# Kernel optimization log

Measured on AMD Instinct MI355X. Metric: run time of the kernel, lower is better.

Reference implementation:

```python
import jax, jax.numpy as jnp
import numpy as np

D_MODEL = 512
N_HEADS = 4  # d_model >= 8 -> 4 heads
HEAD_DIM = D_MODEL // N_HEADS
D_FF = 4 * D_MODEL


def setup_inputs() -> dict:
    key = jax.random.key(0)
    ks = jax.random.split(key, 8)
    B, T = 4, 2048
    s = 0.02
    return {
        "x": jax.random.normal(ks[0], (B, T, D_MODEL), dtype=jnp.float32),
        "ln1_g": jnp.ones((D_MODEL,), jnp.float32),
        "ln1_b": jnp.zeros((D_MODEL,), jnp.float32),
        "w_qkv": jax.random.normal(ks[1], (D_MODEL, 3 * D_MODEL), jnp.float32) * s,
        "w_proj": jax.random.normal(ks[2], (D_MODEL, D_MODEL), jnp.float32) * s,
        "ln2_g": jnp.ones((D_MODEL,), jnp.float32),
        "ln2_b": jnp.zeros((D_MODEL,), jnp.float32),
        "w_ff1": jax.random.normal(ks[3], (D_MODEL, D_FF), jnp.float32) * s,
        "w_ff2": jax.random.normal(ks[4], (D_FF, D_MODEL), jnp.float32) * s,
    }


def _layernorm(x, g, b, eps=1e-5):
    mu = jnp.mean(x, axis=-1, keepdims=True)
    var = jnp.var(x, axis=-1, keepdims=True)
    return (x - mu) * jax.lax.rsqrt(var + eps) * g + b


def _attention(x, w_qkv, w_proj):
    B, T, C = x.shape
    qkv = x @ w_qkv  # [B,T,3C]
    q, k, v = jnp.split(qkv, 3, axis=-1)
    # [B,H,T,Dh]
    q = q.reshape(B, T, N_HEADS, HEAD_DIM).transpose(0, 2, 1, 3)
    k = k.reshape(B, T, N_HEADS, HEAD_DIM).transpose(0, 2, 1, 3)
    v = v.reshape(B, T, N_HEADS, HEAD_DIM).transpose(0, 2, 1, 3)
    scale = 1.0 / jnp.sqrt(jnp.asarray(HEAD_DIM, x.dtype))
    scores = jnp.einsum("bhqd,bhkd->bhqk", q, k) * scale
    causal = jnp.tril(jnp.ones((T, T), bool))
    scores = jnp.where(causal, scores, -jnp.inf)
    attn = jax.nn.softmax(scores, axis=-1)
    out = jnp.einsum("bhqk,bhkd->bhqd", attn, v)
    out = out.transpose(0, 2, 1, 3).reshape(B, T, C)
    return out @ w_proj


def reference(x, ln1_g, ln1_b, w_qkv, w_proj, ln2_g, ln2_b, w_ff1, w_ff2):
    x = x + _attention(_layernorm(x, ln1_g, ln1_b), w_qkv, w_proj)
    h = _layernorm(x, ln2_g, ln2_b)
    h = jax.nn.gelu(h @ w_ff1, approximate=False) @ w_ff2
    return x + h
```

## Files before the change

kernel.cpp:

```cpp
#include <hip/hip_runtime.h>
#include <cstdint>

typedef unsigned short u16;
typedef __attribute__((ext_vector_type(8))) short short8;
typedef __attribute__((ext_vector_type(4))) float floatx4;

#define BT    8192
#define TSEQ  2048
#define NBAT  4
#define CMOD  512
#define NH    4
#define HD    128
#define DFF   2048
#define CQKV  1536

__device__ __forceinline__ u16 f2bf(float f) {
  union { float f; uint32_t u; } v; v.f = f;
  uint32_t r = v.u + 0x7FFFu + ((v.u >> 16) & 1u);
  return (u16)(r >> 16);
}

__device__ __forceinline__ float exp2a(float x) {
  float r; asm("v_exp_f32 %0, %1" : "=v"(r) : "v"(x)); return r;
}
__device__ __forceinline__ float rcpa(float x) {
  float r; asm("v_rcp_f32 %0, %1" : "=v"(r) : "v"(x)); return r;
}

typedef __attribute__((address_space(1))) const unsigned int ga_u32;
typedef __attribute__((address_space(3))) unsigned int ls_u32;
__device__ __forceinline__ void glds16(const u16* g, u16* l) {
  __builtin_amdgcn_global_load_lds((ga_u32*)g, (ls_u32*)l, 16, 0, 0);
}

__global__ __launch_bounds__(256) void transpose_cast(const float* __restrict__ W,
                                                      u16* __restrict__ Wt, int K, int N) {
  __shared__ float tile[32][33];
  int n0 = blockIdx.x * 32, k0 = blockIdx.y * 32;
  int tx = threadIdx.x & 31, ty = threadIdx.x >> 5;
  #pragma unroll
  for (int r = 0; r < 32; r += 8)
    tile[r + ty][tx] = W[(size_t)(k0 + r + ty) * N + n0 + tx];
  __syncthreads();
  #pragma unroll
  for (int r = 0; r < 32; r += 8)
    Wt[(size_t)(n0 + r + ty) * K + k0 + tx] = f2bf(tile[tx][r + ty]);
}

__global__ __launch_bounds__(256) void ln_kernel(const float* __restrict__ x,
                                                 const float* __restrict__ g,
                                                 const float* __restrict__ b,
                                                 u16* __restrict__ out) {
  int row = blockIdx.x * 4 + (threadIdx.x >> 6);
  int lane = threadIdx.x & 63;
  const float4* xr = (const float4*)(x + (size_t)row * CMOD);
  float4 a = xr[lane], c = xr[lane + 64];
  float s = a.x + a.y + a.z + a.w + c.x + c.y + c.z + c.w;
  float q = a.x*a.x + a.y*a.y + a.z*a.z + a.w*a.w
          + c.x*c.x + c.y*c.y + c.z*c.z + c.w*c.w;
  #pragma unroll
  for (int o = 32; o; o >>= 1) { s += __shfl_xor(s, o); q += __shfl_xor(q, o); }
  float mu = s * (1.0f / CMOD);
  float rstd = rsqrtf(q * (1.0f / CMOD) - mu * mu + 1e-5f);
  const float4* gr = (const float4*)g;
  const float4* br = (const float4*)b;
  float4 g0 = gr[lane], g1 = gr[lane + 64], b0 = br[lane], b1 = br[lane + 64];
  u16* orow = out + (size_t)row * CMOD;
  int i0 = lane * 4, i1 = (lane + 64) * 4;
  orow[i0 + 0] = f2bf((a.x - mu) * rstd * g0.x + b0.x);
  orow[i0 + 1] = f2bf((a.y - mu) * rstd * g0.y + b0.y);
  orow[i0 + 2] = f2bf((a.z - mu) * rstd * g0.z + b0.z);
  orow[i0 + 3] = f2bf((a.w - mu) * rstd * g0.w + b0.w);
  orow[i1 + 0] = f2bf((c.x - mu) * rstd * g1.x + b1.x);
  orow[i1 + 1] = f2bf((c.y - mu) * rstd * g1.y + b1.y);
  orow[i1 + 2] = f2bf((c.z - mu) * rstd * g1.z + b1.z);
  orow[i1 + 3] = f2bf((c.w - mu) * rstd * g1.w + b1.w);
}

template <int EPI, int TN>
__global__ __launch_bounds__(256) void gemm_kernel(
    const u16* __restrict__ A, const u16* __restrict__ Bt, int K,
    const float* __restrict__ resid, float* __restrict__ outf,
    u16* __restrict__ ob0, u16* __restrict__ ob1, u16* __restrict__ ob2) {
  constexpr int WNF = TN / 32;
  constexpr int NKB = TN / 64;
  __shared__ __align__(16) u16 As[2][128 * 32];
  __shared__ __align__(16) u16 Bs[2][TN * 32];
  int tid = threadIdx.x;
  int lane = tid & 63, wave = tid >> 6;
  int lane16 = lane & 15, quad = lane >> 4;
  int m0 = blockIdx.y * 128, n0 = blockIdx.x * TN;
  int wm = (wave >> 1) * 64, wn = (wave & 1) * (TN / 2);

  floatx4 acc[4][WNF];
  #pragma unroll
  for (int i = 0; i < 4; i++)
    #pragma unroll
    for (int j = 0; j < WNF; j++) acc[i][j] = (floatx4)(0.0f);

  const u16* agp[2]; u16* alp[2][2];
  const u16* bgp[NKB]; u16* blp[NKB][2];
  #pragma unroll
  for (int i = 0; i < 2; i++) {
    int s = i * 256 + tid;
    agp[i] = A + (size_t)(m0 + (s >> 2)) * K + (s & 3) * 8;
    alp[i][0] = &As[0][(i * 256 + wave * 64) * 8];
    alp[i][1] = &As[1][(i * 256 + wave * 64) * 8];
  }
  #pragma unroll
  for (int i = 0; i < NKB; i++) {
    int s = i * 256 + tid;
    bgp[i] = Bt + (size_t)(n0 + (s >> 2)) * K + (s & 3) * 8;
    blp[i][0] = &Bs[0][(i * 256 + wave * 64) * 8];
    blp[i][1] = &Bs[1][(i * 256 + wave * 64) * 8];
  }

  int nk = K >> 5;
  #pragma unroll
  for (int i = 0; i < 2; i++) glds16(agp[i], alp[i][0]);
  #pragma unroll
  for (int i = 0; i < NKB; i++) glds16(bgp[i], blp[i][0]);

  for (int kt = 0; kt < nk; kt++) {
    __syncthreads();
    int buf = kt & 1;
    if (kt + 1 < nk) {
      int k1 = (kt + 1) * 32;
      #pragma unroll
      for (int i = 0; i < 2; i++) glds16(agp[i] + k1, alp[i][buf ^ 1]);
      #pragma unroll
      for (int i = 0; i < NKB; i++) glds16(bgp[i] + k1, blp[i][buf ^ 1]);
    }
    short8 af[4], bf[WNF];
    #pragma unroll
    for (int i = 0; i < 4; i++)
      af[i] = *(const short8*)&As[buf][(wm + i * 16 + lane16) * 32 + quad * 8];
    #pragma unroll
    for (int j = 0; j < WNF; j++)
      bf[j] = *(const short8*)&Bs[buf][(wn + j * 16 + lane16) * 32 + quad * 8];
    #pragma unroll
    for (int i = 0; i < 4; i++)
      #pragma unroll
      for (int j = 0; j < WNF; j++)
        acc[i][j] = __builtin_amdgcn_mfma_f32_16x16x32_bf16(af[i], bf[j], acc[i][j], 0, 0, 0);
  }

  #pragma unroll
  for (int i = 0; i < 4; i++) {
    #pragma unroll
    for (int j = 0; j < WNF; j++) {
      #pragma unroll
      for (int r = 0; r < 4; r++) {
        int m = m0 + wm + i * 16 + quad * 4 + r;
        int n = n0 + wn + j * 16 + lane16;
        float v = acc[i][j][r];
        if (EPI == 0) {
          int bb = m >> 11, t = m & 2047;
          int nn = n & 511, which = n >> 9;
          int h = nn >> 7, d = nn & 127;
          size_t bh = (size_t)(bb * NH + h);
          if (which == 0)      ob0[bh * TSEQ * HD + (size_t)t * HD + d] = f2bf(v * 0.12751743f);
          else if (which == 1) ob1[bh * TSEQ * HD + (size_t)t * HD + d] = f2bf(v);
          else                 ob2[bh * HD * TSEQ + (size_t)d * TSEQ + t] = f2bf(v);
        } else if (EPI == 1) {
          size_t idx = (size_t)m * CMOD + n;
          outf[idx] = v + resid[idx];
        } else if (EPI == 2) {
          float ge = 0.5f * v * (1.0f + erff(v * 0.70710678118654752f));
          ob0[(size_t)m * DFF + n] = f2bf(ge);
        } else {
          size_t idx = (size_t)m * CMOD + n;
          outf[idx] = v + resid[idx];
        }
      }
    }
  }
}

__global__ __launch_bounds__(256) void attn_kernel(const u16* __restrict__ qb,
                                                   const u16* __restrict__ kb,
                                                   const u16* __restrict__ vtb,
                                                   u16* __restrict__ ob) {
  __shared__ __align__(16) u16 Ks[2][32 * 128];
  __shared__ __align__(16) u16 Vs[2][128 * 32];
  __shared__ __align__(16) uint32_t Ps[4 * 16 * 20];
  int tid = threadIdx.x, wave = tid >> 6, lane = tid & 63;
  int lane16 = lane & 15, quad = lane >> 4;
  int bh = blockIdx.x;
  int qt = 31 - (int)blockIdx.y;
  int q0w = qt * 64 + wave * 16;
  const u16* Q  = qb  + (size_t)bh * TSEQ * HD;
  const u16* Kg = kb  + (size_t)bh * TSEQ * HD;
  const u16* Vg = vtb + (size_t)bh * HD * TSEQ;

  short8 aq[4];
  {
    int qrow = q0w + lane16;
    #pragma unroll
    for (int cc = 0; cc < 4; cc++)
      aq[cc] = *(const short8*)&Q[(size_t)qrow * HD + cc * 32 + quad * 8];
  }

  const u16* kgp[2]; const u16* vgp[2];
  u16* klp[2][2]; u16* vlp[2][2];
  #pragma unroll
  for (int i = 0; i < 2; i++) {
    int s = wave * 128 + i * 64 + lane;
    int r = s >> 4, cp = s & 15, c = cp ^ (r & 7);
    kgp[i] = Kg + (size_t)r * HD + c * 8;
    int d = s >> 2, cv = (s & 3) ^ ((d >> 1) & 3);
    vgp[i] = Vg + (size_t)d * TSEQ + cv * 8;
    #pragma unroll
    for (int bfr = 0; bfr < 2; bfr++) {
      klp[i][bfr] = &Ks[bfr][(wave * 128 + i * 64) * 8];
      vlp[i][bfr] = &Vs[bfr][(wave * 128 + i * 64) * 8];
    }
  }

  int ktw = (q0w >> 5) + 1;
  int ktblk = qt * 2 + 2;

  floatx4 o[8];
  #pragma unroll
  for (int j = 0; j < 8; j++) o[j] = (floatx4)(0.0f);
  floatx4 ol = (floatx4)(0.0f);

  short8 ones;
  #pragma unroll
  for (int e = 0; e < 8; e++) ones[e] = (short)0x3F80;

  uint32_t* Pw = &Ps[wave * 320];
  int swl = lane16 & 7;
  int cvr = quad ^ ((lane16 >> 1) & 3);

  #pragma unroll
  for (int i = 0; i < 2; i++) { glds16(kgp[i], klp[i][0]); glds16(vgp[i], vlp[i][0]); }

  for (int kt = 0; kt < ktblk; kt++) {
    __syncthreads();
    int buf = kt & 1;
    if (kt + 1 < ktblk) {
      int ko = (kt + 1) * 32;
      #pragma unroll
      for (int i = 0; i < 2; i++) {
        glds16(kgp[i] + (size_t)ko * HD, klp[i][buf ^ 1]);
        glds16(vgp[i] + ko, vlp[i][buf ^ 1]);
      }
    }
    if (kt >= ktw) continue;

    floatx4 st0 = (floatx4)(0.0f), st1 = (floatx4)(0.0f);
    #pragma unroll
    for (int cc = 0; cc < 4; cc++) {
      short8 kf0 = *(const short8*)&Ks[buf][(lane16 * 16 + ((cc * 4 + quad) ^ swl)) * 8];
      short8 kf1 = *(const short8*)&Ks[buf][((16 + lane16) * 16 + ((cc * 4 + quad) ^ swl)) * 8];
      st0 = __builtin_amdgcn_mfma_f32_16x16x32_bf16(aq[cc], kf0, st0, 0, 0, 0);
      st1 = __builtin_amdgcn_mfma_f32_16x16x32_bf16(aq[cc], kf1, st1, 0, 0, 0);
    }
    short8 vf[8];
    #pragma unroll
    for (int j = 0; j < 8; j++)
      vf[j] = *(const short8*)&Vs[buf][((j * 16 + lane16) * 4 + cvr) * 8];

    int kg0 = kt * 32 + lane16;
    #pragma unroll
    for (int r = 0; r < 4; r++) {
      int qr = q0w + quad * 4 + r;
      float p0 = exp2a(st0[r]);
      float p1 = exp2a(st1[r]);
      if (kg0 > qr) p0 = 0.0f;
      if (kg0 + 16 > qr) p1 = 0.0f;
      Pw[(quad * 4 + r) * 20 + lane16] =
          __builtin_amdgcn_perm(__float_as_uint(p1), __float_as_uint(p0), 0x07060302u);
    }
    asm volatile("s_waitcnt lgkmcnt(0)" ::: "memory");

    union { uint32_t u[4]; short8 s; } pf;
    {
      const uint32_t* prow = &Pw[lane16 * 20 + (quad & 1) * 8];
      uint32_t d0 = prow[0], d1 = prow[1], d2 = prow[2], d3 = prow[3];
      uint32_t d4 = prow[4], d5 = prow[5], d6 = prow[6], d7 = prow[7];
      uint32_t sel = (quad >> 1) ? 0x07060302u : 0x05040100u;
      pf.u[0] = __builtin_amdgcn_perm(d1, d0, sel);
      pf.u[1] = __builtin_amdgcn_perm(d3, d2, sel);
      pf.u[2] = __builtin_amdgcn_perm(d5, d4, sel);
      pf.u[3] = __builtin_amdgcn_perm(d7, d6, sel);
    }
    #pragma unroll
    for (int j = 0; j < 8; j++)
      o[j] = __builtin_amdgcn_mfma_f32_16x16x32_bf16(pf.s, vf[j], o[j], 0, 0, 0);
    ol = __builtin_amdgcn_mfma_f32_16x16x32_bf16(pf.s, ones, ol, 0, 0, 0);
  }

  int bb = bh >> 2, h = bh & 3;
  #pragma unroll
  for (int r = 0; r < 4; r++) {
    int t = q0w + quad * 4 + r;
    float inv = rcpa(ol[r]);
    #pragma unroll
    for (int j = 0; j < 8; j++)
      ob[((size_t)(bb * TSEQ + t)) * CMOD + h * HD + j * 16 + lane16] = f2bf(o[j][r] * inv);
  }
}

extern "C" void kernel_launch(void* const* d_in, const int* in_sizes, int n_in,
                              void* d_out, int out_size, void* d_ws, size_t ws_size,
                              hipStream_t stream) {
  const float* x     = (const float*)d_in[0];
  const float* ln1g  = (const float*)d_in[1];
  const float* ln1b  = (const float*)d_in[2];
  const float* wqkv  = (const float*)d_in[3];
  const float* wproj = (const float*)d_in[4];
  const float* ln2g  = (const float*)d_in[5];
  const float* ln2b  = (const float*)d_in[6];
  const float* wff1  = (const float*)d_in[7];
  const float* wff2  = (const float*)d_in[8];
  float* out = (float*)d_out;
  char* ws = (char*)d_ws;

  u16* wt_qkv  = (u16*)(ws);
  u16* wt_proj = (u16*)(ws + 1572864);
  u16* wt_ff1  = (u16*)(ws + 2097152);
  u16* wt_ff2  = (u16*)(ws + 4194304);
  u16* ln_buf  = (u16*)(ws + 6291456);
  u16* q_buf   = (u16*)(ws + 14680064);
  u16* k_buf   = (u16*)(ws + 23068672);
  u16* vt_buf  = (u16*)(ws + 31457280);
  u16* attn    = (u16*)(ws + 39845888);
  float* x2    = (float*)(ws + 48234496);
  u16* h1      = (u16*)(ws + 65011712);

  dim3 blk(256);
  transpose_cast<<<dim3(CQKV / 32, CMOD / 32), blk, 0, stream>>>(wqkv, wt_qkv, CMOD, CQKV);
  transpose_cast<<<dim3(CMOD / 32, CMOD / 32), blk, 0, stream>>>(wproj, wt_proj, CMOD, CMOD);
  transpose_cast<<<dim3(DFF / 32, CMOD / 32), blk, 0, stream>>>(wff1, wt_ff1, CMOD, DFF);
  transpose_cast<<<dim3(CMOD / 32, DFF / 32), blk, 0, stream>>>(wff2, wt_ff2, DFF, CMOD);

  ln_kernel<<<dim3(BT / 4), blk, 0, stream>>>(x, ln1g, ln1b, ln_buf);

  gemm_kernel<0, 128><<<dim3(CQKV / 128, BT / 128), blk, 0, stream>>>(
      ln_buf, wt_qkv, CMOD, nullptr, nullptr, q_buf, k_buf, vt_buf);

  attn_kernel<<<dim3(NBAT * NH, TSEQ / 64), blk, 0, stream>>>(q_buf, k_buf, vt_buf, attn);

  gemm_kernel<1, 64><<<dim3(CMOD / 64, BT / 128), blk, 0, stream>>>(
      attn, wt_proj, CMOD, x, x2, nullptr, nullptr, nullptr);

  ln_kernel<<<dim3(BT / 4), blk, 0, stream>>>(x2, ln2g, ln2b, ln_buf);

  gemm_kernel<2, 128><<<dim3(DFF / 128, BT / 128), blk, 0, stream>>>(
      ln_buf, wt_ff1, CMOD, nullptr, nullptr, h1, nullptr, nullptr);

  gemm_kernel<3, 64><<<dim3(CMOD / 64, BT / 128), blk, 0, stream>>>(
      h1, wt_ff2, DFF, x2, out, nullptr, nullptr, nullptr);
}
```

Measured before the change: 285.3 us.

## Split causal attention across KV chunks and merge partials; fuse prep kernels

Attention work for each query tile is split into chunks of up to 16 KV tiles, raising the grid from 32 to 80 blocks per head, so long causal rows no longer serialize on one block. Each chunk writes bf16 partial outputs and row sums, and a new reduce kernel sums them and normalizes. It relies on the exp-based softmax having no running max, so partials can simply be added. The four weight transpose-casts and the first layernorm are merged into one launch to cut launch overhead. The cost is an extra kernel, extra partial-buffer traffic, and bf16 rounding of the partials.

```diff
diff --git a/kernel.cpp b/kernel.cpp
--- a/kernel.cpp
+++ b/kernel.cpp
@@ -19,7 +19,9 @@
   uint32_t r = v.u + 0x7FFFu + ((v.u >> 16) & 1u);
   return (u16)(r >> 16);
 }
-
+__device__ __forceinline__ float bf2f(u16 u) {
+  union { uint32_t u; float f; } v; v.u = ((uint32_t)u) << 16; return v.f;
+}
 __device__ __forceinline__ float exp2a(float x) {
   float r; asm("v_exp_f32 %0, %1" : "=v"(r) : "v"(x)); return r;
 }
@@ -33,11 +35,11 @@
   __builtin_amdgcn_global_load_lds((ga_u32*)g, (ls_u32*)l, 16, 0, 0);
 }
 
-__global__ __launch_bounds__(256) void transpose_cast(const float* __restrict__ W,
-                                                      u16* __restrict__ Wt, int K, int N) {
-  __shared__ float tile[32][33];
-  int n0 = blockIdx.x * 32, k0 = blockIdx.y * 32;
-  int tx = threadIdx.x & 31, ty = threadIdx.x >> 5;
+__device__ __forceinline__ void tcast_body(const float* __restrict__ W, u16* __restrict__ Wt,
+                                           int K, int N, int bx, int by, int tid,
+                                           float (*tile)[33]) {
+  int n0 = bx * 32, k0 = by * 32;
+  int tx = tid & 31, ty = tid >> 5;
   #pragma unroll
   for (int r = 0; r < 32; r += 8)
     tile[r + ty][tx] = W[(size_t)(k0 + r + ty) * N + n0 + tx];
@@ -45,6 +47,50 @@
   #pragma unroll
   for (int r = 0; r < 32; r += 8)
     Wt[(size_t)(n0 + r + ty) * K + k0 + tx] = f2bf(tile[tx][r + ty]);
+}
+
+__global__ __launch_bounds__(256) void prep_kernel(
+    const float* __restrict__ x, const float* __restrict__ g, const float* __restrict__ b,
+    const float* __restrict__ wqkv, const float* __restrict__ wproj,
+    const float* __restrict__ wff1, const float* __restrict__ wff2,
+    u16* __restrict__ ln_out, u16* __restrict__ wqkvT, u16* __restrict__ wprojT,
+    u16* __restrict__ wff1T, u16* __restrict__ wff2T) {
+  __shared__ float tile[32][33];
+  int bid = blockIdx.x, tid = threadIdx.x;
+  if (bid < 768) {
+    tcast_body(wqkv, wqkvT, CMOD, CQKV, bid % 48, bid / 48, tid, tile);
+  } else if (bid < 1024) {
+    int id = bid - 768; tcast_body(wproj, wprojT, CMOD, CMOD, id % 16, id / 16, tid, tile);
+  } else if (bid < 2048) {
+    int id = bid - 1024; tcast_body(wff1, wff1T, CMOD, DFF, id % 64, id / 64, tid, tile);
+  } else if (bid < 3072) {
+    int id = bid - 2048; tcast_body(wff2, wff2T, DFF, CMOD, id % 16, id / 16, tid, tile);
+  } else {
+    int row = (bid - 3072) * 4 + (tid >> 6);
+    int lane = tid & 63;
+    const float4* xr = (const float4*)(x + (size_t)row * CMOD);
+    float4 a = xr[lane], c = xr[lane + 64];
+    float s = a.x + a.y + a.z + a.w + c.x + c.y + c.z + c.w;
+    float q = a.x*a.x + a.y*a.y + a.z*a.z + a.w*a.w
+            + c.x*c.x + c.y*c.y + c.z*c.z + c.w*c.w;
+    #pragma unroll
+    for (int o = 32; o; o >>= 1) { s += __shfl_xor(s, o); q += __shfl_xor(q, o); }
+    float mu = s * (1.0f / CMOD);
+    float rstd = rsqrtf(q * (1.0f / CMOD) - mu * mu + 1e-5f);
+    const float4* gr = (const float4*)g;
+    const float4* br = (const float4*)b;
+    float4 g0 = gr[lane], g1 = gr[lane + 64], b0 = br[lane], b1 = br[lane + 64];
+    u16* orow = ln_out + (size_t)row * CMOD;
+    int i0 = lane * 4, i1 = (lane + 64) * 4;
+    orow[i0 + 0] = f2bf((a.x - mu) * rstd * g0.x + b0.x);
+    orow[i0 + 1] = f2bf((a.y - mu) * rstd * g0.y + b0.y);
+    orow[i0 + 2] = f2bf((a.z - mu) * rstd * g0.z + b0.z);
+    orow[i0 + 3] = f2bf((a.w - mu) * rstd * g0.w + b0.w);
+    orow[i1 + 0] = f2bf((c.x - mu) * rstd * g1.x + b1.x);
+    orow[i1 + 1] = f2bf((c.y - mu) * rstd * g1.y + b1.y);
+    orow[i1 + 2] = f2bf((c.z - mu) * rstd * g1.z + b1.z);
+    orow[i1 + 3] = f2bf((c.w - mu) * rstd * g1.w + b1.w);
+  }
 }
 
 __global__ __launch_bounds__(256) void ln_kernel(const float* __restrict__ x,
@@ -180,14 +226,21 @@
 __global__ __launch_bounds__(256) void attn_kernel(const u16* __restrict__ qb,
                                                    const u16* __restrict__ kb,
                                                    const u16* __restrict__ vtb,
-                                                   u16* __restrict__ ob) {
+                                                   u16* __restrict__ po,
+                                                   float* __restrict__ pl) {
   __shared__ __align__(16) u16 Ks[2][32 * 128];
   __shared__ __align__(16) u16 Vs[2][128 * 32];
   __shared__ __align__(16) uint32_t Ps[4 * 16 * 20];
   int tid = threadIdx.x, wave = tid >> 6, lane = tid & 63;
   int lane16 = lane & 15, quad = lane >> 4;
   int bh = blockIdx.x;
-  int qt = 31 - (int)blockIdx.y;
+  int cid = 79 - (int)blockIdx.y;
+  int qt, c;
+  if (cid < 8)       { qt = cid;                  c = 0; }
+  else if (cid < 24) { qt = 8 + ((cid - 8) >> 1); c = (cid - 8) & 1; }
+  else if (cid < 48) { qt = 16 + (cid - 24) / 3;  c = (cid - 24) % 3; }
+  else               { qt = 24 + ((cid - 48) >> 2); c = (cid - 48) & 3; }
+
   int q0w = qt * 64 + wave * 16;
   const u16* Q  = qb  + (size_t)bh * TSEQ * HD;
   const u16* Kg = kb  + (size_t)bh * TSEQ * HD;
@@ -206,8 +259,8 @@
   #pragma unroll
   for (int i = 0; i < 2; i++) {
     int s = wave * 128 + i * 64 + lane;
-    int r = s >> 4, cp = s & 15, c = cp ^ (r & 7);
-    kgp[i] = Kg + (size_t)r * HD + c * 8;
+    int r = s >> 4, cp = s & 15, cc = cp ^ (r & 7);
+    kgp[i] = Kg + (size_t)r * HD + cc * 8;
     int d = s >> 2, cv = (s & 3) ^ ((d >> 1) & 3);
     vgp[i] = Vg + (size_t)d * TSEQ + cv * 8;
     #pragma unroll
@@ -217,8 +270,10 @@
     }
   }
 
-  int ktw = (q0w >> 5) + 1;
+  int ktw   = (q0w >> 5) + 1;
   int ktblk = qt * 2 + 2;
+  int kt0   = c * 16;
+  int kend  = min(kt0 + 16, ktblk);
 
   floatx4 o[8];
   #pragma unroll
@@ -233,13 +288,19 @@
   int swl = lane16 & 7;
   int cvr = quad ^ ((lane16 >> 1) & 3);
 
-  #pragma unroll
-  for (int i = 0; i < 2; i++) { glds16(kgp[i], klp[i][0]); glds16(vgp[i], vlp[i][0]); }
-
-  for (int kt = 0; kt < ktblk; kt++) {
+  {
+    int ko = kt0 * 32;
+    #pragma unroll
+    for (int i = 0; i < 2; i++) {
+      glds16(kgp[i] + (size_t)ko * HD, klp[i][kt0 & 1]);
+      glds16(vgp[i] + ko, vlp[i][kt0 & 1]);
+    }
+  }
+
+  for (int kt = kt0; kt < kend; kt++) {
     __syncthreads();
     int buf = kt & 1;
-    if (kt + 1 < ktblk) {
+    if (kt + 1 < kend) {
       int ko = (kt + 1) * 32;
       #pragma unroll
       for (int i = 0; i < 2; i++) {
@@ -292,14 +353,51 @@
     ol = __builtin_amdgcn_mfma_f32_16x16x32_bf16(pf.s, ones, ol, 0, 0, 0);
   }
 
-  int bb = bh >> 2, h = bh & 3;
+  int slot = (bh * 32 + qt) * 4 + c;
+  u16* pob = po + (size_t)slot * 8192;
   #pragma unroll
   for (int r = 0; r < 4; r++) {
-    int t = q0w + quad * 4 + r;
-    float inv = rcpa(ol[r]);
+    int qr = wave * 16 + quad * 4 + r;
     #pragma unroll
     for (int j = 0; j < 8; j++)
-      ob[((size_t)(bb * TSEQ + t)) * CMOD + h * HD + j * 16 + lane16] = f2bf(o[j][r] * inv);
+      pob[qr * 128 + j * 16 + lane16] = f2bf(o[j][r]);
+    if (lane16 == 0) pl[slot * 64 + qr] = ol[r];
+  }
+}
+
+__global__ __launch_bounds__(256) void reduce_kernel(const u16* __restrict__ po,
+                                                     const float* __restrict__ pl,
+                                                     u16* __restrict__ attn) {
+  int bh = blockIdx.x >> 5, qt = blockIdx.x & 31;
+  int tid = threadIdx.x;
+  int nch = (2 * qt + 17) >> 4;
+  int qrow = tid >> 2;
+  int d0 = (tid & 3) * 32;
+  float acc[32];
+  #pragma unroll
+  for (int i = 0; i < 32; i++) acc[i] = 0.0f;
+  float l = 0.0f;
+  int slot0 = (bh * 32 + qt) * 4;
+  for (int c = 0; c < nch; c++) {
+    int slot = slot0 + c;
+    l += pl[slot * 64 + qrow];
+    const short8* p = (const short8*)(po + (size_t)slot * 8192 + qrow * 128 + d0);
+    #pragma unroll
+    for (int v = 0; v < 4; v++) {
+      short8 pk = p[v];
+      #pragma unroll
+      for (int e = 0; e < 8; e++) acc[v * 8 + e] += bf2f((u16)pk[e]);
+    }
+  }
+  float inv = rcpa(l);
+  int b = bh >> 2, h = bh & 3, t = qt * 64 + qrow;
+  u16* orow = attn + ((size_t)(b * TSEQ + t)) * CMOD + h * HD + d0;
+  #pragma unroll
+  for (int v = 0; v < 4; v++) {
+    short8 ov;
+    #pragma unroll
+    for (int e = 0; e < 8; e++) ov[e] = (short)f2bf(acc[v * 8 + e] * inv);
+    *(short8*)(orow + v * 8) = ov;
   }
 }
 
@@ -329,19 +427,19 @@
   u16* attn    = (u16*)(ws + 39845888);
   float* x2    = (float*)(ws + 48234496);
   u16* h1      = (u16*)(ws + 65011712);
+  u16* po      = (u16*)(ws + 48234496);
+  float* pl    = (float*)(ws + 81788928);
 
   dim3 blk(256);
-  transpose_cast<<<dim3(CQKV / 32, CMOD / 32), blk, 0, stream>>>(wqkv, wt_qkv, CMOD, CQKV);
-  transpose_cast<<<dim3(CMOD / 32, CMOD / 32), blk, 0, stream>>>(wproj, wt_proj, CMOD, CMOD);
-  transpose_cast<<<dim3(DFF / 32, CMOD / 32), blk, 0, stream>>>(wff1, wt_ff1, CMOD, DFF);
-  transpose_cast<<<dim3(CMOD / 32, DFF / 32), blk, 0, stream>>>(wff2, wt_ff2, DFF, CMOD);
-
-  ln_kernel<<<dim3(BT / 4), blk, 0, stream>>>(x, ln1g, ln1b, ln_buf);
+  prep_kernel<<<dim3(5120), blk, 0, stream>>>(x, ln1g, ln1b, wqkv, wproj, wff1, wff2,
+                                              ln_buf, wt_qkv, wt_proj, wt_ff1, wt_ff2);
 
   gemm_kernel<0, 128><<<dim3(CQKV / 128, BT / 128), blk, 0, stream>>>(
       ln_buf, wt_qkv, CMOD, nullptr, nullptr, q_buf, k_buf, vt_buf);
 
-  attn_kernel<<<dim3(NBAT * NH, TSEQ / 64), blk, 0, stream>>>(q_buf, k_buf, vt_buf, attn);
+  attn_kernel<<<dim3(NBAT * NH, 80), blk, 0, stream>>>(q_buf, k_buf, vt_buf, po, pl);
+
+  reduce_kernel<<<dim3(512), blk, 0, stream>>>(po, pl, attn);
 
   gemm_kernel<1, 64><<<dim3(CMOD / 64, BT / 128), blk, 0, stream>>>(
       attn, wt_proj, CMOD, x, x2, nullptr, nullptr, nullptr);
```

After: 276.7 us. -3.0%, faster.
